# Kernel optimization log

Measured on AMD Instinct MI355X. Metric: run time of the kernel, lower is better.

Reference implementation:

```python
import jax, jax.numpy as jnp
import numpy as np

N_NODES = 8192
N_EDGES = 81920
N_EDGE2 = 1310720
D_EMB = 128
D_GAT = 64
H = 128
N_CLASSES = 2


def setup_inputs() -> dict:
    key = jax.random.key(0)
    ks = jax.random.split(key, 18)
    s = 0.05
    return {
        "x": jax.random.normal(ks[0], (N_NODES, D_EMB), jnp.float32),
        "embed": jax.random.normal(ks[1], (N_NODES, D_EMB), jnp.float32),
        "noise": jax.random.uniform(ks[2], (N_EDGES,), jnp.float32, 1e-6, 1.0 - 1e-6),
        "tmp": jnp.ones((), jnp.float32),
        "gat_W": jax.random.normal(ks[3], (2 * D_EMB, D_GAT), jnp.float32) * s,
        "att_src": jax.random.normal(ks[4], (D_GAT,), jnp.float32) * s,
        "att_dst": jax.random.normal(ks[5], (D_GAT,), jnp.float32) * s,
        "gat_bias": jax.random.normal(ks[6], (D_GAT,), jnp.float32) * s,
        "lin_W": jax.random.normal(ks[7], (D_GAT, 1), jnp.float32) * s,
        "lin_b": jax.random.normal(ks[8], (1,), jnp.float32) * s,
        "W1": jax.random.normal(ks[9], (D_EMB, H), jnp.float32) * s,
        "W2": jax.random.normal(ks[10], (H, H), jnp.float32) * s,
        "W3": jax.random.normal(ks[11], (H, H), jnp.float32) * s,
        "Wc": jax.random.normal(ks[12], (H, N_CLASSES), jnp.float32) * s,
        "edge_index": jax.random.randint(ks[13], (2, N_EDGES), 0, N_NODES, jnp.int32),
        "new_edge_index": jax.random.randint(ks[14], (2, N_EDGE2), 0, N_EDGES, jnp.int32),
        "label": 1,
    }


def reference(x, embed, noise, tmp, gat_W, att_src, att_dst, gat_bias, lin_W, lin_b,
              W1, W2, W3, Wc, edge_index, new_edge_index, label):
    N, E = x.shape[0], edge_index.shape[1]
    row, col = edge_index[0], edge_index[1]

    # h = cat(embed[row], embed[col])  -> [E, 2D]
    h = jnp.concatenate([embed[row], embed[col]], axis=-1)

    # --- GATConv(2D, 64) over the edge-adjacency graph (PyG single-head, self-loops) ---
    hp = h @ gat_W                              # [E, D_GAT]
    a_s = hp @ att_src                          # [E]
    a_d = hp @ att_dst                          # [E]
    loop = jnp.arange(E, dtype=new_edge_index.dtype)
    src = jnp.concatenate([new_edge_index[0], loop])
    dst = jnp.concatenate([new_edge_index[1], loop])
    alpha = jax.nn.leaky_relu(a_s[src] + a_d[dst], negative_slope=0.2)
    amax = jax.ops.segment_max(alpha, dst, num_segments=E)
    ealpha = jnp.exp(alpha - amax[dst])
    denom = jax.ops.segment_sum(ealpha, dst, num_segments=E)
    attn = ealpha / denom[dst]                  # softmax per destination edge-node
    gat_out = jax.ops.segment_sum(attn[:, None] * hp[src], dst, num_segments=E) + gat_bias

    # Linear(64, 1)
    log_alpha = (gat_out @ lin_W + lin_b).reshape(-1)   # [E]

    # concrete_sample (training=True, sample_bias=0.0)
    gate = jax.nn.sigmoid((jnp.log(noise) - jnp.log1p(-noise) + log_alpha) / tmp)

    # dense adjacency (ones, coalesce-sum) and dense gated mask
    adj = jnp.zeros((N, N), jnp.float32).at[row, col].add(1.0)
    sym_mask = jnp.zeros((N, N), jnp.float32).at[row, col].add(gate)
    sym_mask = (sym_mask + sym_mask.T) * 0.5
    masked_adj = adj * sym_mask
    edge_mask = masked_adj[row, col]

    # --- stub downstream model: 3-layer edge-weighted GCN + mean pool + classifier ---
    # explain-mode edge masking: messages weighted by sigmoid(edge_mask)
    w = jax.nn.sigmoid(edge_mask)
    deg = jax.ops.segment_sum(w, col, num_segments=N) + 1.0   # [N]

    def gcn(xh, W):
        msg = jax.ops.segment_sum(w[:, None] * xh[row], col, num_segments=N)
        return jax.nn.relu(((xh + msg) / deg[:, None]) @ W)

    h1 = gcn(x, W1)
    h2 = gcn(h1, W2)
    h3 = gcn(h2, W3)
    g = h3.mean(axis=0)                         # global mean pool (single graph)
    logits = g @ Wc
    return jax.nn.softmax(logits, axis=-1)
```

## Files before the change

### kernel.cpp

```cpp
#include <hip/hip_runtime.h>
#include <hip/hip_fp16.h>
#include <math.h>

typedef unsigned long long u64;

#define NN 8192
#define EE 81920
#define E2C 1310720
#define HSZ (1 << 18)
#define HMASK (HSZ - 1)
#define NBIN 320
#define BCAP 4800
#define SBITS 17

__device__ __forceinline__ float wsum(float v) {
#pragma unroll
  for (int m = 32; m > 0; m >>= 1) v += __shfl_xor(v, m, 64);
  return v;
}
__device__ __forceinline__ float lrelu(float x) { return x > 0.f ? x : 0.2f * x; }
__device__ __forceinline__ unsigned packh2(float a, float b) {
  __half2 h = __floats2half2_rn(a, b);
  return *reinterpret_cast<unsigned*>(&h);
}
__device__ __forceinline__ void atomic_pk_add_f16(unsigned* addr, unsigned data) {
  asm volatile("global_atomic_pk_add_f16 %0, %1, off" :: "v"(addr), "v"(data) : "memory");
}
__device__ __forceinline__ int hfind(const int* __restrict__ keys, int key) {
  unsigned i = ((unsigned)key * 2654435761u) >> 14 & HMASK;
  while (true) {
    int k = keys[i];
    if (k == key) return (int)i;
    if (k == -1) return -1;
    i = (i + 1) & HMASK;
  }
}
__device__ __forceinline__ float2 bf2f(unsigned u) {
  return make_float2(__uint_as_float(u << 16), __uint_as_float(u & 0xffff0000u));
}
__device__ __forceinline__ unsigned f2bf(float a, float b) {
  unsigned ua = __float_as_uint(a);
  ua = (ua + 0x7fffu + ((ua >> 16) & 1u)) >> 16;
  unsigned ub = __float_as_uint(b);
  ub = ((ub + 0x7fffu + ((ub >> 16) & 1u)) >> 16) << 16;
  return (ua & 0xffffu) | ub;
}

__global__ __launch_bounds__(256) void kA(const float* __restrict__ x,
                                          const float* __restrict__ embed,
                                          const float* __restrict__ gw,
                                          const float* __restrict__ att_s,
                                          const float* __restrict__ att_d,
                                          const float* __restrict__ lin_W,
                                          float4* __restrict__ pN, float4* __restrict__ qN,
                                          unsigned* __restrict__ xb,
                                          int* __restrict__ hKeys, unsigned* __restrict__ hPair,
                                          int* __restrict__ colCnt, float* __restrict__ gvec,
                                          unsigned* __restrict__ done, unsigned* __restrict__ gCur) {
  __shared__ float sm[768];
  int t = threadIdx.x, bid = blockIdx.x;
  int lane = t & 63, wv = t >> 6;
  for (int i = bid * 256 + t; i < HSZ; i += 512 * 256) { hKeys[i] = -1; hPair[i] = 0u; }
  for (int i = bid * 256 + t; i < NN; i += 512 * 256) colCnt[i] = 0;
  if (bid == 0) {
    if (t < 128) gvec[t] = 0.f;
    if (t == 0) *done = 0u;
    for (int i = t; i < NBIN; i += 256) gCur[i] = 0u;
  }
  {
    const float4* x4 = (const float4*)x;
    float4 a = x4[bid * 512 + t * 2];
    float4 b = x4[bid * 512 + t * 2 + 1];
    uint4 o;
    o.x = f2bf(a.x, a.y); o.y = f2bf(a.z, a.w);
    o.z = f2bf(b.x, b.y); o.w = f2bf(b.z, b.w);
    ((uint4*)xb)[bid * 256 + t] = o;
  }
  {
    float sa = 0.f, sd = 0.f, sz = 0.f;
#pragma unroll 8
    for (int k = 0; k < 64; k++) {
      float w = gw[t * 64 + k];
      sa += w * att_s[k]; sd += w * att_d[k]; sz += w * lin_W[k];
    }
    sm[t] = sa; sm[256 + t] = sd; sm[512 + t] = sz;
  }
  __syncthreads();
#pragma unroll
  for (int j = 0; j < 4; j++) {
    int n = bid * 16 + wv * 4 + j;
    float e0 = embed[n * 128 + lane], e1 = embed[n * 128 + 64 + lane];
    float pA = wsum(e0 * sm[lane] + e1 * sm[64 + lane]);
    float qA = wsum(e0 * sm[128 + lane] + e1 * sm[192 + lane]);
    float pD = wsum(e0 * sm[256 + lane] + e1 * sm[320 + lane]);
    float qD = wsum(e0 * sm[384 + lane] + e1 * sm[448 + lane]);
    float pZ = wsum(e0 * sm[512 + lane] + e1 * sm[576 + lane]);
    float qZ = wsum(e0 * sm[640 + lane] + e1 * sm[704 + lane]);
    if (lane == 0) pN[n] = make_float4(pA, pD, pZ, 0.f);
    if (lane == 1) qN[n] = make_float4(qA, qD, qZ, 0.f);
  }
}

__global__ void kB(const int* __restrict__ row, const int* __restrict__ col,
                   const float4* __restrict__ pN, const float4* __restrict__ qN,
                   float2* __restrict__ asz, float* __restrict__ ad, int* __restrict__ colCnt) {
  int e = blockIdx.x * 256 + threadIdx.x;
  int r = row[e], c = col[e];
  float4 p = pN[r];
  float4 q = qN[c];
  asz[e] = make_float2(p.x + q.x, p.z + q.z);
  ad[e] = p.y + q.y;
  atomicAdd(&colCnt[c], 1);
}

__global__ __launch_bounds__(256) void kC(const int* __restrict__ src2, const int* __restrict__ dst2,
                                          const int* __restrict__ colCnt, int* __restrict__ colOffs,
                                          int* __restrict__ colCur,
                                          unsigned* __restrict__ gCur, unsigned* __restrict__ bucket) {
  int t = threadIdx.x;
  if (blockIdx.x == 320) {
    __shared__ int sd32[256];
    int beg = t * 32;
    int s = 0;
#pragma unroll 8
    for (int i = 0; i < 32; i++) s += colCnt[beg + i];
    sd32[t] = s;
    __syncthreads();
    for (int o = 1; o < 256; o <<= 1) {
      int v = (t >= o) ? sd32[t - o] : 0;
      __syncthreads();
      sd32[t] += v;
      __syncthreads();
    }
    int run = (t == 0) ? 0 : sd32[t - 1];
    for (int i = 0; i < 32; i++) {
      colOffs[beg + i] = run;
      colCur[beg + i] = run;
      run += colCnt[beg + i];
    }
    if (t == 255) colOffs[NN] = run;
    return;
  }
  __shared__ unsigned hist[NBIN], base[NBIN], lcur[NBIN];
  for (int i = t; i < NBIN; i += 256) { hist[i] = 0u; lcur[i] = 0u; }
  __syncthreads();
  int blockBase = blockIdx.x * 4096;
  int4 dv[4];
#pragma unroll
  for (int j = 0; j < 4; j++) {
    dv[j] = *(const int4*)&dst2[blockBase + j * 1024 + t * 4];
    atomicAdd(&hist[dv[j].x >> 8], 1u);
    atomicAdd(&hist[dv[j].y >> 8], 1u);
    atomicAdd(&hist[dv[j].z >> 8], 1u);
    atomicAdd(&hist[dv[j].w >> 8], 1u);
  }
  __syncthreads();
  for (int i = t; i < NBIN; i += 256)
    if (hist[i]) base[i] = atomicAdd(&gCur[i], hist[i]);
  __syncthreads();
#pragma unroll
  for (int j = 0; j < 4; j++) {
    int4 sv = *(const int4*)&src2[blockBase + j * 1024 + t * 4];
    int ss[4] = {sv.x, sv.y, sv.z, sv.w};
    int dd[4] = {dv[j].x, dv[j].y, dv[j].z, dv[j].w};
#pragma unroll
    for (int k = 0; k < 4; k++) {
      int s = ss[k], d = dd[k];
      int b = d >> 8;
      unsigned r = atomicAdd(&lcur[b], 1u);
      unsigned pos = base[b] + r;
      if (pos < BCAP) bucket[(size_t)b * BCAP + pos] = ((unsigned)(d & 255) << SBITS) | (unsigned)s;
    }
  }
}

__global__ __launch_bounds__(256) void kD(const int* __restrict__ row, const int* __restrict__ col,
                                          const float2* __restrict__ asz, const float* __restrict__ ad,
                                          const unsigned* __restrict__ bucket, const unsigned* __restrict__ gCur,
                                          const float* __restrict__ gat_b, const float* __restrict__ lin_W,
                                          const float* __restrict__ lin_b, const float* __restrict__ noise,
                                          const float* __restrict__ tmp,
                                          int* __restrict__ hKeys, unsigned* __restrict__ hPair) {
  __shared__ float acc[512];
  __shared__ float adl[256];
  int b = blockIdx.x, t = threadIdx.x, lane = t & 63;
  acc[2 * t] = 0.f; acc[2 * t + 1] = 0.f; adl[t] = ad[b * 256 + t];
  __syncthreads();
  int cnt = min((int)gCur[b], BCAP);
  const unsigned* bp = bucket + (size_t)b * BCAP;
  const unsigned SM = (1u << SBITS) - 1;
  int i = t;
  for (; i + 768 < cnt; i += 1024) {
    unsigned u0 = bp[i], u1 = bp[i + 256], u2 = bp[i + 512], u3 = bp[i + 768];
    float2 az0 = asz[u0 & SM], az1 = asz[u1 & SM], az2 = asz[u2 & SM], az3 = asz[u3 & SM];
    int l0 = u0 >> SBITS, l1 = u1 >> SBITS, l2 = u2 >> SBITS, l3 = u3 >> SBITS;
    float ea0 = __expf(lrelu(az0.x + adl[l0]));
    float ea1 = __expf(lrelu(az1.x + adl[l1]));
    float ea2 = __expf(lrelu(az2.x + adl[l2]));
    float ea3 = __expf(lrelu(az3.x + adl[l3]));
    atomicAdd(&acc[2 * l0], ea0); atomicAdd(&acc[2 * l0 + 1], ea0 * az0.y);
    atomicAdd(&acc[2 * l1], ea1); atomicAdd(&acc[2 * l1 + 1], ea1 * az1.y);
    atomicAdd(&acc[2 * l2], ea2); atomicAdd(&acc[2 * l2 + 1], ea2 * az2.y);
    atomicAdd(&acc[2 * l3], ea3); atomicAdd(&acc[2 * l3 + 1], ea3 * az3.y);
  }
  for (; i < cnt; i += 256) {
    unsigned u = bp[i];
    float2 az = asz[u & SM];
    int l = u >> SBITS;
    float ea = __expf(lrelu(az.x + adl[l]));
    atomicAdd(&acc[2 * l], ea);
    atomicAdd(&acc[2 * l + 1], ea * az.y);
  }
  __syncthreads();
  float gb = wsum(gat_b[lane] * lin_W[lane]) + lin_b[0];
  float itmp = 1.f / tmp[0];
  {
    int e = b * 256 + t;
    float2 szv = asz[e];
    float eself = __expf(lrelu(szv.x + adl[t]));
    float la = (acc[2 * t + 1] + eself * szv.y) / (acc[2 * t] + eself) + gb;
    float ns = noise[e];
    float g = (logf(ns) - log1pf(-ns) + la) * itmp;
    float gate = 1.f / (1.f + __expf(-g));
    int key = row[e] * NN + col[e];
    unsigned hi = ((unsigned)key * 2654435761u) >> 14 & HMASK;
    while (true) {
      int old = atomicCAS(&hKeys[hi], -1, key);
      if (old == -1 || old == key) break;
      hi = (hi + 1) & HMASK;
    }
    atomic_pk_add_f16(&hPair[hi], packh2(1.0f, gate));
  }
}

__global__ void kE(const int* __restrict__ row, const int* __restrict__ col,
                   const int* __restrict__ hKeys, const unsigned* __restrict__ hPair,
                   int* __restrict__ colCur, int2* __restrict__ csrP) {
  int e = blockIdx.x * 256 + threadIdx.x;
  int r = row[e], c = col[e];
  int s1 = hfind(hKeys, r * NN + c);
  unsigned u1 = hPair[s1];
  __half2 h1 = *reinterpret_cast<__half2*>(&u1);
  float cv = __low2float(h1), g1 = __high2float(h1);
  int s2 = hfind(hKeys, c * NN + r);
  float g2 = 0.f;
  if (s2 >= 0) {
    unsigned u2 = hPair[s2];
    g2 = __high2float(*reinterpret_cast<__half2*>(&u2));
  }
  float em = cv * 0.5f * (g1 + g2);
  float w = 1.f / (1.f + __expf(-em));
  int pos = atomicAdd(&colCur[c], 1);
  csrP[pos] = make_int2(r, __float_as_int(w));
}

__device__ __forceinline__ float2 gatherNode(const unsigned* __restrict__ xb, int n, int lane,
                                             const int* __restrict__ colOffs,
                                             const int2* __restrict__ csrP) {
  float2 sf = bf2f(xb[n * 64 + lane]);
  float a0 = sf.x, a1 = sf.y, ws = 0.f;
  int off = colOffs[n], end = colOffs[n + 1];
  int i = off;
  for (; i + 4 <= end; i += 4) {
    int2 q0 = csrP[i], q1 = csrP[i + 1], q2 = csrP[i + 2], q3 = csrP[i + 3];
    unsigned u0 = xb[q0.x * 64 + lane];
    unsigned u1 = xb[q1.x * 64 + lane];
    unsigned u2 = xb[q2.x * 64 + lane];
    unsigned u3 = xb[q3.x * 64 + lane];
    float w0 = __int_as_float(q0.y), w1 = __int_as_float(q1.y);
    float w2 = __int_as_float(q2.y), w3 = __int_as_float(q3.y);
    ws += w0 + w1 + w2 + w3;
    float2 f0 = bf2f(u0), f1 = bf2f(u1), f2v = bf2f(u2), f3 = bf2f(u3);
    a0 += w0 * f0.x + w1 * f1.x + w2 * f2v.x + w3 * f3.x;
    a1 += w0 * f0.y + w1 * f1.y + w2 * f2v.y + w3 * f3.y;
  }
  for (; i < end; i++) {
    int2 q = csrP[i];
    unsigned u = xb[q.x * 64 + lane];
    float w = __int_as_float(q.y);
    ws += w;
    float2 f = bf2f(u);
    a0 += w * f.x;
    a1 += w * f.y;
  }
  float inv = 1.f / (1.f + ws);
  return make_float2(a0 * inv, a1 * inv);
}

__global__ __launch_bounds__(256) void kF(const unsigned* __restrict__ xb,
                                          const int* __restrict__ colOffs,
                                          const int2* __restrict__ csrP,
                                          const float* __restrict__ W,
                                          unsigned* __restrict__ outB) {
  __shared__ unsigned Wl[128 * 64];
  __shared__ float Tl[16 * 128];
  int t = threadIdx.x;
  const float4* W4 = (const float4*)W;
  for (int i = t; i < 4096; i += 256) {
    float4 a = W4[i];
    ((uint2*)Wl)[i] = make_uint2(f2bf(a.x, a.y), f2bf(a.z, a.w));
  }
  int lane = t & 63, wv = t >> 6;
  int nb = blockIdx.x * 16;
#pragma unroll
  for (int j = 0; j < 4; j++) {
    int n = nb + wv * 4 + j;
    float2 tv = gatherNode(xb, n, lane, colOffs, csrP);
    ((float2*)Tl)[(wv * 4 + j) * 64 + lane] = tv;
  }
  __syncthreads();
  float2 acc[4];
#pragma unroll
  for (int j = 0; j < 4; j++) acc[j] = make_float2(0.f, 0.f);
  for (int k = 0; k < 128; k++) {
    float2 w2 = bf2f(Wl[k * 64 + lane]);
#pragma unroll
    for (int j = 0; j < 4; j++) {
      float tv = Tl[(wv * 4 + j) * 128 + k];
      acc[j].x += tv * w2.x;
      acc[j].y += tv * w2.y;
    }
  }
#pragma unroll
  for (int j = 0; j < 4; j++) {
    int n = nb + wv * 4 + j;
    outB[n * 64 + lane] = f2bf(fmaxf(acc[j].x, 0.f), fmaxf(acc[j].y, 0.f));
  }
}

__global__ __launch_bounds__(256) void kH(const unsigned* __restrict__ xb,
                                          const int* __restrict__ colOffs,
                                          const int2* __restrict__ csrP,
                                          const float* __restrict__ W,
                                          const float* __restrict__ Wc,
                                          float* __restrict__ gvec, unsigned* __restrict__ done,
                                          float* __restrict__ out) {
  __shared__ unsigned Wl[128 * 64];
  __shared__ float Tl[16 * 128];
  __shared__ unsigned lastFlag;
  int t = threadIdx.x;
  const float4* W4 = (const float4*)W;
  for (int i = t; i < 4096; i += 256) {
    float4 a = W4[i];
    ((uint2*)Wl)[i] = make_uint2(f2bf(a.x, a.y), f2bf(a.z, a.w));
  }
  int lane = t & 63, wv = t >> 6;
  int nb = blockIdx.x * 16;
#pragma unroll
  for (int j = 0; j < 4; j++) {
    int n = nb + wv * 4 + j;
    float2 tv = gatherNode(xb, n, lane, colOffs, csrP);
    ((float2*)Tl)[(wv * 4 + j) * 64 + lane] = tv;
  }
  __syncthreads();
  float2 acc[4];
#pragma unroll
  for (int j = 0; j < 4; j++) acc[j] = make_float2(0.f, 0.f);
  for (int k = 0; k < 128; k++) {
    float2 w2 = bf2f(Wl[k * 64 + lane]);
#pragma unroll
    for (int j = 0; j < 4; j++) {
      float tv = Tl[(wv * 4 + j) * 128 + k];
      acc[j].x += tv * w2.x;
      acc[j].y += tv * w2.y;
    }
  }
  float s0 = 0.f, s1 = 0.f;
#pragma unroll
  for (int j = 0; j < 4; j++) {
    s0 += fmaxf(acc[j].x, 0.f);
    s1 += fmaxf(acc[j].y, 0.f);
  }
  __syncthreads();
  float* gpart = Tl;
  if (t < 128) gpart[t] = 0.f;
  __syncthreads();
  atomicAdd(&gpart[2 * lane], s0);
  atomicAdd(&gpart[2 * lane + 1], s1);
  __syncthreads();
  if (t < 128) atomicAdd(&gvec[t], gpart[t]);
  __threadfence();
  __syncthreads();
  if (t == 0) lastFlag = (atomicAdd(done, 1u) == gridDim.x - 1) ? 1u : 0u;
  __syncthreads();
  if (lastFlag) {
    float* f0 = Tl + 256;
    float* f1 = Tl + 384;
    if (t < 128) {
      float gj = atomicAdd(&gvec[t], 0.f) * (1.0f / 8192.0f);
      f0[t] = gj * Wc[t * 2 + 0];
      f1[t] = gj * Wc[t * 2 + 1];
    }
    __syncthreads();
    for (int o = 64; o > 0; o >>= 1) {
      if (t < o) { f0[t] += f0[t + o]; f1[t] += f1[t + o]; }
      __syncthreads();
    }
    if (t == 0) {
      float l0 = f0[0], l1 = f1[0];
      float m = fmaxf(l0, l1);
      float e0 = __expf(l0 - m), e1 = __expf(l1 - m);
      float inv = 1.f / (e0 + e1);
      out[0] = e0 * inv;
      out[1] = e1 * inv;
    }
  }
}

extern "C" void kernel_launch(void* const* d_in, const int* in_sizes, int n_in,
                              void* d_out, int out_size, void* d_ws, size_t ws_size,
                              hipStream_t stream) {
  const float* x     = (const float*)d_in[0];
  const float* embed = (const float*)d_in[1];
  const float* noise = (const float*)d_in[2];
  const float* tmp   = (const float*)d_in[3];
  const float* gat_W = (const float*)d_in[4];
  const float* att_s = (const float*)d_in[5];
  const float* att_d = (const float*)d_in[6];
  const float* gat_b = (const float*)d_in[7];
  const float* lin_W = (const float*)d_in[8];
  const float* lin_b = (const float*)d_in[9];
  const float* W1    = (const float*)d_in[10];
  const float* W2    = (const float*)d_in[11];
  const float* W3    = (const float*)d_in[12];
  const float* Wc    = (const float*)d_in[13];
  const int* ei      = (const int*)d_in[14];
  const int* nei     = (const int*)d_in[15];
  const int* row = ei;
  const int* col = ei + EE;
  const int* src2 = nei;
  const int* dst2 = nei + E2C;
  float* out = (float*)d_out;

  char* w8 = (char*)d_ws;
  size_t off = 0;
  auto alloc = [&](size_t units) -> void* {
    void* p = w8 + off * 4;
    off += units;
    return p;
  };
  float4*   pN      = (float4*)alloc(4 * NN);
  float4*   qN      = (float4*)alloc(4 * NN);
  float2*   asz     = (float2*)alloc(2 * EE);
  int2*     csrP    = (int2*)alloc(2 * EE);
  unsigned* xb      = (unsigned*)alloc(NN * 64);
  unsigned* H1b     = (unsigned*)alloc(NN * 64);
  unsigned* H2b     = (unsigned*)alloc(NN * 64);
  float*    ad      = (float*)alloc(EE);
  int*      colCnt  = (int*)alloc(NN);
  int*      colOffs = (int*)alloc(NN + 2);
  int*      colCur  = (int*)alloc(NN);
  int*      hKeys   = (int*)alloc(HSZ);
  unsigned* hPair   = (unsigned*)alloc(HSZ);
  unsigned* bucket  = (unsigned*)alloc((size_t)NBIN * BCAP);
  unsigned* gCur    = (unsigned*)alloc(NBIN);
  float*    gvec    = (float*)alloc(128);
  unsigned* done    = (unsigned*)alloc(2);

  kA<<<512, 256, 0, stream>>>(x, embed, gat_W, att_s, att_d, lin_W, pN, qN, xb,
                              hKeys, hPair, colCnt, gvec, done, gCur);
  kB<<<EE / 256, 256, 0, stream>>>(row, col, pN, qN, asz, ad, colCnt);
  kC<<<321, 256, 0, stream>>>(src2, dst2, colCnt, colOffs, colCur, gCur, bucket);
  kD<<<NBIN, 256, 0, stream>>>(row, col, asz, ad, bucket, gCur, gat_b, lin_W,
                               lin_b, noise, tmp, hKeys, hPair);
  kE<<<EE / 256, 256, 0, stream>>>(row, col, hKeys, hPair, colCur, csrP);
  kF<<<NN / 16, 256, 0, stream>>>(xb, colOffs, csrP, W1, H1b);
  kF<<<NN / 16, 256, 0, stream>>>(H1b, colOffs, csrP, W2, H2b);
  kH<<<NN / 16, 256, 0, stream>>>(H2b, colOffs, csrP, W3, Wc, gvec, done, out);
}
```

Before: 249.1 us.

## Gather GCN messages edge-parallel per block with LDS atomics and shuffle-based matmul

The per-node CSR gather, where each wave walked the in-edges of its own four nodes, becomes an edge-parallel sweep over the block's contiguous 16-node edge range. The local destination index is packed into the CSR entry's high bits, and messages and weight sums are accumulated through shared-memory float atomics. This balances work across waves when in-degree varies. The dense transform now keeps W transposed in padded LDS and broadcasts activations with shuffles. The last-block fence is replaced by s_waitcnt, which adds LDS atomic contention and a weaker memory-ordering guarantee.

```diff
diff --git a/kernel.cpp b/kernel.cpp
--- a/kernel.cpp
+++ b/kernel.cpp
@@ -12,6 +12,8 @@
 #define NBIN 320
 #define BCAP 4800
 #define SBITS 17
+#define WST 129
+#define TST 130
 
 __device__ __forceinline__ float wsum(float v) {
 #pragma unroll
@@ -251,76 +253,92 @@
   float em = cv * 0.5f * (g1 + g2);
   float w = 1.f / (1.f + __expf(-em));
   int pos = atomicAdd(&colCur[c], 1);
-  csrP[pos] = make_int2(r, __float_as_int(w));
-}
-
-__device__ __forceinline__ float2 gatherNode(const unsigned* __restrict__ xb, int n, int lane,
-                                             const int* __restrict__ colOffs,
-                                             const int2* __restrict__ csrP) {
-  float2 sf = bf2f(xb[n * 64 + lane]);
-  float a0 = sf.x, a1 = sf.y, ws = 0.f;
-  int off = colOffs[n], end = colOffs[n + 1];
-  int i = off;
-  for (; i + 4 <= end; i += 4) {
-    int2 q0 = csrP[i], q1 = csrP[i + 1], q2 = csrP[i + 2], q3 = csrP[i + 3];
-    unsigned u0 = xb[q0.x * 64 + lane];
-    unsigned u1 = xb[q1.x * 64 + lane];
-    unsigned u2 = xb[q2.x * 64 + lane];
-    unsigned u3 = xb[q3.x * 64 + lane];
-    float w0 = __int_as_float(q0.y), w1 = __int_as_float(q1.y);
-    float w2 = __int_as_float(q2.y), w3 = __int_as_float(q3.y);
-    ws += w0 + w1 + w2 + w3;
-    float2 f0 = bf2f(u0), f1 = bf2f(u1), f2v = bf2f(u2), f3 = bf2f(u3);
-    a0 += w0 * f0.x + w1 * f1.x + w2 * f2v.x + w3 * f3.x;
-    a1 += w0 * f0.y + w1 * f1.y + w2 * f2v.y + w3 * f3.y;
-  }
-  for (; i < end; i++) {
-    int2 q = csrP[i];
-    unsigned u = xb[q.x * 64 + lane];
-    float w = __int_as_float(q.y);
-    ws += w;
-    float2 f = bf2f(u);
-    a0 += w * f.x;
-    a1 += w * f.y;
-  }
-  float inv = 1.f / (1.f + ws);
-  return make_float2(a0 * inv, a1 * inv);
-}
+  csrP[pos] = make_int2(r | ((c & 15) << 16), __float_as_int(w));
+}
+
+#define LAYER_BODY(XB, NB)                                                          \
+  {                                                                                 \
+    for (int i = t; i < 4096; i += 256) {              \
+      float4 a = W4[i];                                                             \
+      int k = i >> 5, o2 = (i & 31) * 2;                                            \
+      Wl[o2 * WST + k] = f2bf(a.x, a.y);                                            \
+      Wl[(o2 + 1) * WST + k] = f2bf(a.z, a.w);                                      \
+    }                                                                               \
+    for (int i = t; i < 16 * TST; i += 256) Tacc[i] = 0.f;                          \
+    if (t < 16) wsAcc[t] = 0.f;                                                     \
+    if (t < 17) offsL[t] = colOffs[(NB) + t];                                       \
+    __syncthreads();                                                                \
+    int beg = offsL[0], endE = offsL[16];                                           \
+    int e = beg + (wv << 2);                                                        \
+    for (; e + 3 < endE; e += 16) {                                                 \
+      int2 q0 = csrP[e], q1 = csrP[e + 1], q2 = csrP[e + 2], q3 = csrP[e + 3];      \
+      unsigned u0 = (XB)[(q0.x & 0xffff) * 64 + lane];                              \
+      unsigned u1 = (XB)[(q1.x & 0xffff) * 64 + lane];                              \
+      unsigned u2 = (XB)[(q2.x & 0xffff) * 64 + lane];                              \
+      unsigned u3 = (XB)[(q3.x & 0xffff) * 64 + lane];                              \
+      float w0 = __int_as_float(q0.y), w1 = __int_as_float(q1.y);                   \
+      float w2 = __int_as_float(q2.y), w3 = __int_as_float(q3.y);                   \
+      int n0 = q0.x >> 16, n1 = q1.x >> 16, n2 = q2.x >> 16, n3 = q3.x >> 16;       \
+      float2 f0 = bf2f(u0), f1 = bf2f(u1), f2v = bf2f(u2), f3 = bf2f(u3);           \
+      atomicAdd(&Tacc[n0 * TST + 2 * lane], w0 * f0.x);                             \
+      atomicAdd(&Tacc[n0 * TST + 2 * lane + 1], w0 * f0.y);                         \
+      atomicAdd(&Tacc[n1 * TST + 2 * lane], w1 * f1.x);                             \
+      atomicAdd(&Tacc[n1 * TST + 2 * lane + 1], w1 * f1.y);                         \
+      atomicAdd(&Tacc[n2 * TST + 2 * lane], w2 * f2v.x);                            \
+      atomicAdd(&Tacc[n2 * TST + 2 * lane + 1], w2 * f2v.y);                        \
+      atomicAdd(&Tacc[n3 * TST + 2 * lane], w3 * f3.x);                             \
+      atomicAdd(&Tacc[n3 * TST + 2 * lane + 1], w3 * f3.y);                         \
+      if (lane == 0) {                                                              \
+        atomicAdd(&wsAcc[n0], w0); atomicAdd(&wsAcc[n1], w1);                       \
+        atomicAdd(&wsAcc[n2], w2); atomicAdd(&wsAcc[n3], w3);                       \
+      }                                                                             \
+    }                                                                               \
+    for (int ee = e; ee < min(e + 4, endE); ee++) {                                 \
+      int2 q = csrP[ee];                                                            \
+      unsigned u = (XB)[(q.x & 0xffff) * 64 + lane];                                \
+      float w = __int_as_float(q.y);                                                \
+      int nl = q.x >> 16;                                                           \
+      float2 f = bf2f(u);                                                           \
+      atomicAdd(&Tacc[nl * TST + 2 * lane], w * f.x);                               \
+      atomicAdd(&Tacc[nl * TST + 2 * lane + 1], w * f.y);                           \
+      if (lane == 0) atomicAdd(&wsAcc[nl], w);                                      \
+    }                                                                               \
+    __syncthreads();                                                                \
+    float2 tv[4];                                                                   \
+    _Pragma("unroll") for (int j = 0; j < 4; j++) {                                 \
+      int nl = wv * 4 + j;                                                          \
+      float2 sf = bf2f((XB)[((NB) + nl) * 64 + lane]);                              \
+      float inv = 1.f / (1.f + wsAcc[nl]);                                          \
+      tv[j].x = (sf.x + Tacc[nl * TST + 2 * lane]) * inv;                           \
+      tv[j].y = (sf.y + Tacc[nl * TST + 2 * lane + 1]) * inv;                       \
+    }                                                                               \
+    _Pragma("unroll") for (int j = 0; j < 4; j++) acc[j] = make_float2(0.f, 0.f);   \
+    _Pragma("unroll 8") for (int k2 = 0; k2 < 64; k2++) {                           \
+      float2 w0 = bf2f(Wl[lane * WST + 2 * k2]);                                    \
+      float2 w1 = bf2f(Wl[lane * WST + 2 * k2 + 1]);                                \
+      _Pragma("unroll") for (int j = 0; j < 4; j++) {                               \
+        float bx = __shfl(tv[j].x, k2, 64);                                         \
+        float by = __shfl(tv[j].y, k2, 64);                                         \
+        acc[j].x += bx * w0.x + by * w1.x;                                          \
+        acc[j].y += bx * w0.y + by * w1.y;                                          \
+      }                                                                             \
+    }                                                                               \
+  }
 
 __global__ __launch_bounds__(256) void kF(const unsigned* __restrict__ xb,
                                           const int* __restrict__ colOffs,
                                           const int2* __restrict__ csrP,
                                           const float* __restrict__ W,
                                           unsigned* __restrict__ outB) {
-  __shared__ unsigned Wl[128 * 64];
-  __shared__ float Tl[16 * 128];
-  int t = threadIdx.x;
+  __shared__ unsigned Wl[128 * WST];
+  __shared__ float Tacc[16 * TST];
+  __shared__ float wsAcc[16];
+  __shared__ int offsL[17];
+  int t = threadIdx.x, lane = t & 63, wv = t >> 6;
+  int nb = blockIdx.x * 16;
   const float4* W4 = (const float4*)W;
-  for (int i = t; i < 4096; i += 256) {
-    float4 a = W4[i];
-    ((uint2*)Wl)[i] = make_uint2(f2bf(a.x, a.y), f2bf(a.z, a.w));
-  }
-  int lane = t & 63, wv = t >> 6;
-  int nb = blockIdx.x * 16;
-#pragma unroll
-  for (int j = 0; j < 4; j++) {
-    int n = nb + wv * 4 + j;
-    float2 tv = gatherNode(xb, n, lane, colOffs, csrP);
-    ((float2*)Tl)[(wv * 4 + j) * 64 + lane] = tv;
-  }
-  __syncthreads();
   float2 acc[4];
-#pragma unroll
-  for (int j = 0; j < 4; j++) acc[j] = make_float2(0.f, 0.f);
-  for (int k = 0; k < 128; k++) {
-    float2 w2 = bf2f(Wl[k * 64 + lane]);
-#pragma unroll
-    for (int j = 0; j < 4; j++) {
-      float tv = Tl[(wv * 4 + j) * 128 + k];
-      acc[j].x += tv * w2.x;
-      acc[j].y += tv * w2.y;
-    }
-  }
+  LAYER_BODY(xb, nb)
 #pragma unroll
   for (int j = 0; j < 4; j++) {
     int n = nb + wv * 4 + j;
@@ -335,36 +353,16 @@
                                           const float* __restrict__ Wc,
                                           float* __restrict__ gvec, unsigned* __restrict__ done,
                                           float* __restrict__ out) {
-  __shared__ unsigned Wl[128 * 64];
-  __shared__ float Tl[16 * 128];
+  __shared__ unsigned Wl[128 * WST];
+  __shared__ float Tacc[16 * TST];
+  __shared__ float wsAcc[16];
+  __shared__ int offsL[17];
   __shared__ unsigned lastFlag;
-  int t = threadIdx.x;
+  int t = threadIdx.x, lane = t & 63, wv = t >> 6;
+  int nb = blockIdx.x * 16;
   const float4* W4 = (const float4*)W;
-  for (int i = t; i < 4096; i += 256) {
-    float4 a = W4[i];
-    ((uint2*)Wl)[i] = make_uint2(f2bf(a.x, a.y), f2bf(a.z, a.w));
-  }
-  int lane = t & 63, wv = t >> 6;
-  int nb = blockIdx.x * 16;
-#pragma unroll
-  for (int j = 0; j < 4; j++) {
-    int n = nb + wv * 4 + j;
-    float2 tv = gatherNode(xb, n, lane, colOffs, csrP);
-    ((float2*)Tl)[(wv * 4 + j) * 64 + lane] = tv;
-  }
-  __syncthreads();
   float2 acc[4];
-#pragma unroll
-  for (int j = 0; j < 4; j++) acc[j] = make_float2(0.f, 0.f);
-  for (int k = 0; k < 128; k++) {
-    float2 w2 = bf2f(Wl[k * 64 + lane]);
-#pragma unroll
-    for (int j = 0; j < 4; j++) {
-      float tv = Tl[(wv * 4 + j) * 128 + k];
-      acc[j].x += tv * w2.x;
-      acc[j].y += tv * w2.y;
-    }
-  }
+  LAYER_BODY(xb, nb)
   float s0 = 0.f, s1 = 0.f;
 #pragma unroll
   for (int j = 0; j < 4; j++) {
@@ -372,20 +370,20 @@
     s1 += fmaxf(acc[j].y, 0.f);
   }
   __syncthreads();
-  float* gpart = Tl;
+  float* gpart = Tacc;
   if (t < 128) gpart[t] = 0.f;
   __syncthreads();
   atomicAdd(&gpart[2 * lane], s0);
   atomicAdd(&gpart[2 * lane + 1], s1);
   __syncthreads();
   if (t < 128) atomicAdd(&gvec[t], gpart[t]);
-  __threadfence();
+  asm volatile("s_waitcnt vmcnt(0)" ::: "memory");
   __syncthreads();
   if (t == 0) lastFlag = (atomicAdd(done, 1u) == gridDim.x - 1) ? 1u : 0u;
   __syncthreads();
   if (lastFlag) {
-    float* f0 = Tl + 256;
-    float* f1 = Tl + 384;
+    float* f0 = Tacc + 256;
+    float* f1 = Tacc + 384;
     if (t < 128) {
       float gj = atomicAdd(&gvec[t], 0.f) * (1.0f / 8192.0f);
       f0[t] = gj * Wc[t * 2 + 0];
```

New measurement: 406.8 us. 63.3% more time.

## Use register readlane broadcast in GCN GEMM and halve nodes per block

Applied to the files above, without the earlier changes.

The GCN layer kernels no longer stage gathered node features in shared memory. Each wave keeps its two nodes' aggregated features in registers and broadcasts individual k elements with readlane during the 128x128 matmul. Each block now handles 8 nodes instead of 16, doubling the grid and freeing LDS. The last-block detection in kH now reuses the weight LDS buffer and replaces the threadfence with an explicit vmcnt wait, which may weaken cross-block visibility ordering. Weight conversion to bf16 in LDS is now repeated in twice as many blocks.

```diff
diff --git a/kernel.cpp b/kernel.cpp
--- a/kernel.cpp
+++ b/kernel.cpp
@@ -44,6 +44,9 @@
   unsigned ub = __float_as_uint(b);
   ub = ((ub + 0x7fffu + ((ub >> 16) & 1u)) >> 16) << 16;
   return (ua & 0xffffu) | ub;
+}
+__device__ __forceinline__ float rdlane(float v, int k) {
+  return __uint_as_float(__builtin_amdgcn_readlane(__float_as_uint(v), k));
 }
 
 __global__ __launch_bounds__(256) void kA(const float* __restrict__ x,
@@ -287,43 +290,44 @@
   return make_float2(a0 * inv, a1 * inv);
 }
 
+#define GEMM2(tv, acc)                                                   \
+  {                                                                      \
+    _Pragma("unroll") for (int j = 0; j < 2; j++) acc[j] = make_float2(0.f, 0.f); \
+    _Pragma("unroll 16") for (int k2 = 0; k2 < 64; k2++) {               \
+      float2 w0 = bf2f(Wl[(2 * k2) * 64 + lane]);                        \
+      float2 w1 = bf2f(Wl[(2 * k2 + 1) * 64 + lane]);                    \
+      _Pragma("unroll") for (int j = 0; j < 2; j++) {                    \
+        float bx = rdlane(tv[j].x, k2);                                  \
+        float by = rdlane(tv[j].y, k2);                                  \
+        acc[j].x += bx * w0.x + by * w1.x;                               \
+        acc[j].y += bx * w0.y + by * w1.y;                               \
+      }                                                                  \
+    }                                                                    \
+  }
+
 __global__ __launch_bounds__(256) void kF(const unsigned* __restrict__ xb,
                                           const int* __restrict__ colOffs,
                                           const int2* __restrict__ csrP,
                                           const float* __restrict__ W,
                                           unsigned* __restrict__ outB) {
   __shared__ unsigned Wl[128 * 64];
-  __shared__ float Tl[16 * 128];
-  int t = threadIdx.x;
+  int t = threadIdx.x, lane = t & 63, wv = t >> 6;
   const float4* W4 = (const float4*)W;
   for (int i = t; i < 4096; i += 256) {
     float4 a = W4[i];
     ((uint2*)Wl)[i] = make_uint2(f2bf(a.x, a.y), f2bf(a.z, a.w));
   }
-  int lane = t & 63, wv = t >> 6;
-  int nb = blockIdx.x * 16;
-#pragma unroll
-  for (int j = 0; j < 4; j++) {
-    int n = nb + wv * 4 + j;
-    float2 tv = gatherNode(xb, n, lane, colOffs, csrP);
-    ((float2*)Tl)[(wv * 4 + j) * 64 + lane] = tv;
-  }
-  __syncthreads();
-  float2 acc[4];
-#pragma unroll
-  for (int j = 0; j < 4; j++) acc[j] = make_float2(0.f, 0.f);
-  for (int k = 0; k < 128; k++) {
-    float2 w2 = bf2f(Wl[k * 64 + lane]);
-#pragma unroll
-    for (int j = 0; j < 4; j++) {
-      float tv = Tl[(wv * 4 + j) * 128 + k];
-      acc[j].x += tv * w2.x;
-      acc[j].y += tv * w2.y;
-    }
-  }
-#pragma unroll
-  for (int j = 0; j < 4; j++) {
-    int n = nb + wv * 4 + j;
+  int nb = blockIdx.x * 8;
+  float2 tv[2];
+#pragma unroll
+  for (int j = 0; j < 2; j++)
+    tv[j] = gatherNode(xb, nb + wv * 2 + j, lane, colOffs, csrP);
+  __syncthreads();
+  float2 acc[2];
+  GEMM2(tv, acc)
+#pragma unroll
+  for (int j = 0; j < 2; j++) {
+    int n = nb + wv * 2 + j;
     outB[n * 64 + lane] = f2bf(fmaxf(acc[j].x, 0.f), fmaxf(acc[j].y, 0.f));
   }
 }
@@ -336,56 +340,38 @@
                                           float* __restrict__ gvec, unsigned* __restrict__ done,
                                           float* __restrict__ out) {
   __shared__ unsigned Wl[128 * 64];
-  __shared__ float Tl[16 * 128];
-  __shared__ unsigned lastFlag;
-  int t = threadIdx.x;
+  int t = threadIdx.x, lane = t & 63, wv = t >> 6;
   const float4* W4 = (const float4*)W;
   for (int i = t; i < 4096; i += 256) {
     float4 a = W4[i];
     ((uint2*)Wl)[i] = make_uint2(f2bf(a.x, a.y), f2bf(a.z, a.w));
   }
-  int lane = t & 63, wv = t >> 6;
-  int nb = blockIdx.x * 16;
-#pragma unroll
-  for (int j = 0; j < 4; j++) {
-    int n = nb + wv * 4 + j;
-    float2 tv = gatherNode(xb, n, lane, colOffs, csrP);
-    ((float2*)Tl)[(wv * 4 + j) * 64 + lane] = tv;
-  }
-  __syncthreads();
-  float2 acc[4];
-#pragma unroll
-  for (int j = 0; j < 4; j++) acc[j] = make_float2(0.f, 0.f);
-  for (int k = 0; k < 128; k++) {
-    float2 w2 = bf2f(Wl[k * 64 + lane]);
-#pragma unroll
-    for (int j = 0; j < 4; j++) {
-      float tv = Tl[(wv * 4 + j) * 128 + k];
-      acc[j].x += tv * w2.x;
-      acc[j].y += tv * w2.y;
-    }
-  }
-  float s0 = 0.f, s1 = 0.f;
-#pragma unroll
-  for (int j = 0; j < 4; j++) {
-    s0 += fmaxf(acc[j].x, 0.f);
-    s1 += fmaxf(acc[j].y, 0.f);
-  }
-  __syncthreads();
-  float* gpart = Tl;
+  int nb = blockIdx.x * 8;
+  float2 tv[2];
+#pragma unroll
+  for (int j = 0; j < 2; j++)
+    tv[j] = gatherNode(xb, nb + wv * 2 + j, lane, colOffs, csrP);
+  __syncthreads();
+  float2 acc[2];
+  GEMM2(tv, acc)
+  float s0 = fmaxf(acc[0].x, 0.f) + fmaxf(acc[1].x, 0.f);
+  float s1 = fmaxf(acc[0].y, 0.f) + fmaxf(acc[1].y, 0.f);
+  __syncthreads();
+  float* gpart = (float*)Wl;
+  unsigned* flagp = (unsigned*)Wl + 600;
   if (t < 128) gpart[t] = 0.f;
   __syncthreads();
   atomicAdd(&gpart[2 * lane], s0);
   atomicAdd(&gpart[2 * lane + 1], s1);
   __syncthreads();
   if (t < 128) atomicAdd(&gvec[t], gpart[t]);
-  __threadfence();
-  __syncthreads();
-  if (t == 0) lastFlag = (atomicAdd(done, 1u) == gridDim.x - 1) ? 1u : 0u;
-  __syncthreads();
-  if (lastFlag) {
-    float* f0 = Tl + 256;
-    float* f1 = Tl + 384;
+  asm volatile("s_waitcnt vmcnt(0)" ::: "memory");
+  __syncthreads();
+  if (t == 0) *flagp = (atomicAdd(done, 1u) == gridDim.x - 1) ? 1u : 0u;
+  __syncthreads();
+  if (*flagp) {
+    float* f0 = (float*)Wl + 256;
+    float* f1 = (float*)Wl + 384;
     if (t < 128) {
       float gj = atomicAdd(&gvec[t], 0.f) * (1.0f / 8192.0f);
       f0[t] = gj * Wc[t * 2 + 0];
@@ -464,7 +450,7 @@
   kD<<<NBIN, 256, 0, stream>>>(row, col, asz, ad, bucket, gCur, gat_b, lin_W,
                                lin_b, noise, tmp, hKeys, hPair);
   kE<<<EE / 256, 256, 0, stream>>>(row, col, hKeys, hPair, colCur, csrP);
-  kF<<<NN / 16, 256, 0, stream>>>(xb, colOffs, csrP, W1, H1b);
-  kF<<<NN / 16, 256, 0, stream>>>(H1b, colOffs, csrP, W2, H2b);
-  kH<<<NN / 16, 256, 0, stream>>>(H2b, colOffs, csrP, W3, Wc, gvec, done, out);
-}
+  kF<<<NN / 8, 256, 0, stream>>>(xb, colOffs, csrP, W1, H1b);
+  kF<<<NN / 8, 256, 0, stream>>>(H1b, colOffs, csrP, W2, H2b);
+  kH<<<NN / 8, 256, 0, stream>>>(H2b, colOffs, csrP, W3, Wc, gvec, done, out);
+}
```

After: 248.7 us. Within noise of the previous version (-0.1%).
